# Kernel optimization log

Measured on AMD Instinct MI355X. Metric: run time of the kernel, lower is better.

Reference implementation:

```python
import jax, jax.numpy as jnp
import numpy as np

V, E, HID, K, S = 100000, 256, 512, 20, 4096
HD = HID // 2  # per-direction LSTM hidden
START_ID, STOP_ID = 18, 19


def setup_inputs() -> dict:
    key = jax.random.key(0)
    ks = jax.random.split(key, 14)
    sentence = jax.random.randint(ks[0], (S,), 0, V)
    tags = jax.random.randint(ks[1], (S,), 0, START_ID)  # real tags only
    embed = jax.random.normal(ks[2], (V, E), jnp.float32) * 0.1
    w_ih_f = jax.random.normal(ks[3], (4 * HD, E), jnp.float32) * 0.05
    w_hh_f = jax.random.normal(ks[4], (4 * HD, HD), jnp.float32) * 0.05
    b_f = jax.random.normal(ks[5], (4 * HD,), jnp.float32) * 0.05
    w_ih_b = jax.random.normal(ks[6], (4 * HD, E), jnp.float32) * 0.05
    w_hh_b = jax.random.normal(ks[7], (4 * HD, HD), jnp.float32) * 0.05
    b_b = jax.random.normal(ks[8], (4 * HD,), jnp.float32) * 0.05
    h0 = jax.random.normal(ks[9], (2, HD), jnp.float32)
    c0 = jax.random.normal(ks[10], (2, HD), jnp.float32)
    emit_W = jax.random.normal(ks[11], (K, HID), jnp.float32) * 0.05
    emit_b = jax.random.normal(ks[12], (K,), jnp.float32) * 0.05
    transition = jax.random.normal(ks[13], (K, K), jnp.float32)
    transition = transition.at[START_ID, :].set(-10000.0)
    transition = transition.at[:, STOP_ID].set(-10000.0)
    return dict(sentence=sentence, tags=tags, embed=embed,
                w_ih_f=w_ih_f, w_hh_f=w_hh_f, b_f=b_f,
                w_ih_b=w_ih_b, w_hh_b=w_hh_b, b_b=b_b,
                h0=h0, c0=c0, emit_W=emit_W, emit_b=emit_b,
                transition=transition)


def _lstm_scan(xs, w_ih, w_hh, b, h, c):
    # xs: (S, E); torch gate order i, f, g, o
    def step(carry, x):
        h, c = carry
        z = x @ w_ih.T + h @ w_hh.T + b  # (4*HD,)
        i, f, g, o = jnp.split(z, 4)
        i, f, o = jax.nn.sigmoid(i), jax.nn.sigmoid(f), jax.nn.sigmoid(o)
        g = jnp.tanh(g)
        c = f * c + i * g
        h = o * jnp.tanh(c)
        return (h, c), h
    _, hs = jax.lax.scan(step, (h, c), xs)
    return hs  # (S, HD)


def reference(sentence, tags, embed, w_ih_f, w_hh_f, b_f,
              w_ih_b, w_hh_b, b_b, h0, c0, emit_W, emit_b, transition):
    xs = embed[sentence]  # (S, E)
    h_fwd = _lstm_scan(xs, w_ih_f, w_hh_f, b_f, h0[0], c0[0])
    h_bwd = _lstm_scan(xs[::-1], w_ih_b, w_hh_b, b_b, h0[1], c0[1])[::-1]
    feats = jnp.concatenate([h_fwd, h_bwd], axis=-1) @ emit_W.T + emit_b  # (S, K)

    # CRF forward algorithm (log-partition), tag dim fully vectorized.
    init_fv = jnp.full((K,), -10000.0, feats.dtype).at[START_ID].set(0.0)

    def crf_step(fv, feat):
        # fv_new[next] = logsumexp_prev(fv[prev] + T[next, prev] + feat[next])
        fv = jax.scipy.special.logsumexp(fv[None, :] + transition + feat[:, None], axis=1)
        return fv, None

    fv, _ = jax.lax.scan(crf_step, init_fv, feats)
    log_z = jax.scipy.special.logsumexp(fv + transition[STOP_ID])

    # Gold path score.
    tags_ext = jnp.concatenate([jnp.array([START_ID], tags.dtype), tags])
    gold = (transition[tags_ext[1:], tags_ext[:-1]].sum()
            + feats[jnp.arange(S), tags].sum()
            + transition[STOP_ID, tags[-1]])
    return jnp.stack([log_z, gold])
```

## Files before the change

kernel.cpp:

```cpp
#include <hip/hip_runtime.h>
#include <stdint.h>

#define SLEN 4096
#define EDIM 256
#define HD 256
#define G4 1024
#define KT 20
#define START_ID 18
#define STOP_ID 19

#define NVC 23
#define NLC 9
#define LSTM_LDS_BYTES (1024 + 1024 * NLC * 16)

typedef _Float16 half_t;
typedef _Float16 half2_t __attribute__((ext_vector_type(2)));

__device__ __forceinline__ float dot2(uint32_t w, uint32_t h, float acc) {
#if __has_builtin(__builtin_amdgcn_fdot2)
    return __builtin_amdgcn_fdot2(__builtin_bit_cast(half2_t, w),
                                  __builtin_bit_cast(half2_t, h), acc, false);
#else
    half2_t wv = __builtin_bit_cast(half2_t, w);
    half2_t hv = __builtin_bit_cast(half2_t, h);
    acc += (float)wv.x * (float)hv.x;
    acc += (float)wv.y * (float)hv.y;
    return acc;
#endif
}

__device__ __forceinline__ float fsig(float x) { return 1.f / (1.f + __expf(-x)); }
__device__ __forceinline__ float ftanh(float x) { return 1.f - 2.f / (__expf(2.f * x) + 1.f); }


__global__ __launch_bounds__(256) void k_transpose_ih(const float* __restrict__ wf,
                                                      const float* __restrict__ wb,
                                                      float* __restrict__ wT) {
    __shared__ float tile[32][33];
    int d = blockIdx.z;
    const float* w = d ? wb : wf;
    int ob = blockIdx.x * 32;
    int eb = blockIdx.y * 32;
    int tx = threadIdx.x & 31, ty = threadIdx.x >> 5;
#pragma unroll
    for (int r = 0; r < 32; r += 8)
        tile[ty + r][tx] = w[(long)(ob + ty + r) * EDIM + eb + tx];
    __syncthreads();
    float* dst = wT + (long)d * EDIM * G4;
#pragma unroll
    for (int r = 0; r < 32; r += 8)
        dst[(long)(eb + ty + r) * G4 + ob + tx] = tile[tx][ty + r];
}

__global__ __launch_bounds__(1024) void k_pack_hh(const float* __restrict__ whf,
                                                  const float* __restrict__ whb,
                                                  uint32_t* __restrict__ wpack,
                                                  uint32_t* __restrict__ wtail) {
    int d = blockIdx.y;
    const float* W = d ? whb : whf;
    int t = threadIdx.x;
    int wv = t >> 6, l = t & 63;
    int j = (wv << 4) | (l & 15);
    int g = (l >> 4) & 3;
    int o = g * 256 + j;
    int bx = blockIdx.x;
    if (bx < 92) {
        int k = bx * 2;
        half2_t p = {(half_t)W[(long)o * HD + k], (half_t)W[(long)o * HD + k + 1]};
        wpack[(d * 92 + bx) * 1024 + t] = __builtin_bit_cast(uint32_t, p);
    } else {
        int cb = bx - 92;
        uint32_t q[4];
#pragma unroll
        for (int qq = 0; qq < 4; qq++) {
            int k = 2 * (92 + cb * 4 + qq);
            half2_t p = {(half_t)W[(long)o * HD + k], (half_t)W[(long)o * HD + k + 1]};
            q[qq] = __builtin_bit_cast(uint32_t, p);
        }
        uint4* dst = (uint4*)wtail;
        dst[(d * NLC + cb) * 1024 + t] = make_uint4(q[0], q[1], q[2], q[3]);
    }
}

__global__ __launch_bounds__(256) void k_zx(const int* __restrict__ sentence,
                                            const float* __restrict__ embed,
                                            const float* __restrict__ wT,
                                            const float* __restrict__ bf,
                                            const float* __restrict__ bb,
                                            float* __restrict__ zxp) {
    int d = blockIdx.y;
    int s0 = blockIdx.x * 16;
    const float* bias = d ? bb : bf;
    __shared__ float xbuf[16][EDIM];
    int tid = threadIdx.x;
    for (int r = 0; r < 16; r++) {
        int row = sentence[s0 + r];
        xbuf[r][tid] = embed[(long)row * EDIM + tid];
    }
    __syncthreads();
    const float* wTd = wT + (long)d * EDIM * G4;
    for (int og = 0; og < 4; og++) {
        float acc[16];
#pragma unroll
        for (int r = 0; r < 16; r++) acc[r] = 0.f;
        int o = og * 256 + tid;
        for (int e = 0; e < EDIM; e += 4) {
            float w0 = wTd[(long)(e + 0) * G4 + o];
            float w1 = wTd[(long)(e + 1) * G4 + o];
            float w2 = wTd[(long)(e + 2) * G4 + o];
            float w3 = wTd[(long)(e + 3) * G4 + o];
#pragma unroll
            for (int r = 0; r < 16; r++) {
                float4 x4 = *(const float4*)&xbuf[r][e];
                acc[r] += w0 * x4.x + w1 * x4.y + w2 * x4.z + w3 * x4.w;
            }
        }
        float bv = bias[o];
        int tB = ((tid >> 4) << 6) | (og << 4) | (tid & 15);
#pragma unroll
        for (int r = 0; r < 16; r++)
            zxp[(long)(d * SLEN + s0 + r) * G4 + tB] = acc[r] + bv;
    }
}

__global__ __launch_bounds__(1024, 4) void k_lstm(const float* __restrict__ zxp,
                                                  const uint32_t* __restrict__ wpack,
                                                  const uint4* __restrict__ wtail,
                                                  const float* __restrict__ h0,
                                                  const float* __restrict__ c0,
                                                  float* __restrict__ hs) {
    extern __shared__ char smem[];
    uint4* h2q = (uint4*)smem;
    half_t* h2h = (half_t*)smem;
    uint4* tail = (uint4*)(smem + 1024);

    int d = blockIdx.x;
    int t = threadIdx.x;
    int l = t & 63;
    int j = ((t >> 6) << 4) | (l & 15);

    uint32_t wreg[4 * NVC];
#pragma unroll
    for (int kk = 0; kk < 4 * NVC; kk++) wreg[kk] = wpack[(d * 92 + kk) * 1024 + t];

#pragma unroll
    for (int cb = 0; cb < NLC; cb++)
        tail[cb * 1024 + t] = wtail[(d * NLC + cb) * 1024 + t];

    float c = c0[d * HD + j];
    if (t < 128) {
        half2_t p = {(half_t)h0[d * HD + 2 * t], (half_t)h0[d * HD + 2 * t + 1]};
        ((uint32_t*)h2q)[t] = __builtin_bit_cast(uint32_t, p);
    }
    __syncthreads();

    const float* zxd = zxp + (long)d * SLEN * G4 + t;
    float* hsd = hs + (long)d * SLEN * HD + j;

    float zx_next = zxd[(long)(d ? SLEN - 1 : 0) * G4];

    for (int s = 0; s < SLEN; s++) {
        const int p = s & 1;
        float zx = zx_next;
        if (s + 1 < SLEN) {
            int sxn = d ? (SLEN - 2 - s) : (s + 1);
            zx_next = zxd[(long)sxn * G4];
        }
        const uint4* hq = h2q + p * 32;
        float acc0 = 0.f, acc1 = 0.f;
#pragma unroll
        for (int cc = 0; cc < NVC; cc++) {
            uint4 hv = hq[cc];
            acc0 = dot2(wreg[4 * cc + 0], hv.x, acc0);
            acc1 = dot2(wreg[4 * cc + 1], hv.y, acc1);
            acc0 = dot2(wreg[4 * cc + 2], hv.z, acc0);
            acc1 = dot2(wreg[4 * cc + 3], hv.w, acc1);
        }
#pragma unroll
        for (int cb = 0; cb < NLC; cb++) {
            uint4 tw = tail[cb * 1024 + t];
            uint4 hv = hq[NVC + cb];
            acc0 = dot2(tw.x, hv.x, acc0);
            acc1 = dot2(tw.y, hv.y, acc1);
            acc0 = dot2(tw.z, hv.z, acc0);
            acc1 = dot2(tw.w, hv.w, acc1);
        }
        float z = acc0 + acc1 + zx;
        int lj = l & 15;
        float zi = __shfl(z, lj, 64);
        float zf = __shfl(z, lj + 16, 64);
        float zg = __shfl(z, lj + 32, 64);
        float zo = __shfl(z, lj + 48, 64);
        float ig = fsig(zi), fg = fsig(zf), og = fsig(zo);
        float gg = ftanh(zg);
        c = fg * c + ig * gg;
        float hval = og * ftanh(c);
        if (l < 16) {
            int sx = d ? (SLEN - 1 - s) : s;
            hsd[(long)sx * HD] = hval;
            h2h[((p ^ 1) << 8) + j] = (half_t)hval;
        }
        __syncthreads();
    }
}

__global__ __launch_bounds__(192) void k_feats(const float* __restrict__ hs,
                                               const float* __restrict__ emitW,
                                               const float* __restrict__ emitb,
                                               float* __restrict__ feats) {
    __shared__ float wb[KT][516];
    __shared__ float hb[8][516];
    int tid = threadIdx.x;
    int s0 = blockIdx.x * 8;
    for (int idx = tid; idx < KT * 512; idx += 192) {
        wb[idx >> 9][idx & 511] = emitW[idx];
    }
    for (int idx = tid; idx < 8 * 512; idx += 192) {
        int sl = idx >> 9, jj = idx & 511;
        float v = (jj < 256) ? hs[(long)(s0 + sl) * HD + jj]
                             : hs[(long)(SLEN + s0 + sl) * HD + (jj - 256)];
        hb[sl][jj] = v;
    }
    __syncthreads();
    if (tid < 160) {
        int sl = tid / KT, k = tid % KT;
        float acc = emitb[k];
        for (int jj = 0; jj < 512; jj += 4) {
            float4 wv = *(const float4*)&wb[k][jj];
            float4 hv = *(const float4*)&hb[sl][jj];
            acc += wv.x * hv.x + wv.y * hv.y + wv.z * hv.z + wv.w * hv.w;
        }
        feats[(long)(s0 + sl) * KT + k] = acc;
    }
}

__global__ __launch_bounds__(256) void k_gold(const float* __restrict__ feats,
                                              const int* __restrict__ tags,
                                              const float* __restrict__ trans,
                                              float* __restrict__ out) {
    __shared__ float red[256];
    int tid = threadIdx.x;
    float local = 0.f;
    for (int s2 = tid; s2 < SLEN; s2 += 256) {
        int cur = tags[s2];
        int prev = s2 ? tags[s2 - 1] : START_ID;
        local += trans[cur * KT + prev] + feats[(long)s2 * KT + cur];
    }
    red[tid] = local;
    __syncthreads();
    for (int off = 128; off; off >>= 1) {
        if (tid < off) red[tid] += red[tid + off];
        __syncthreads();
    }
    if (tid == 0) out[1] = red[0] + trans[STOP_ID * KT + tags[SLEN - 1]];
}

__global__ __launch_bounds__(512) void k_crf_chunk(const float* __restrict__ feats,
                                                   const float* __restrict__ trans,
                                                   float* __restrict__ mats) {
    __shared__ float T[KT][KT + 1];
    __shared__ float fb[16][KT];
    __shared__ float cur[2][KT][KT + 1];
    int tid = threadIdx.x;
    int t0 = blockIdx.x * 16;
    if (tid < KT * KT) T[tid / KT][tid % KT] = trans[tid];
    for (int idx = tid; idx < 16 * KT; idx += 512) fb[idx / KT][idx % KT] = feats[(long)t0 * KT + idx];
    __syncthreads();
    int i = tid / KT, jc = tid % KT;
    bool act = tid < KT * KT;
    if (act) cur[0][i][jc] = T[i][jc] + fb[0][i];
    __syncthreads();
    for (int m = 1; m < 16; m++) {
        int p = (m - 1) & 1;
        float nv = 0.f;
        if (act) {
            float vs[KT], vmax = -1e30f;
#pragma unroll
            for (int k = 0; k < KT; k++) { vs[k] = T[i][k] + cur[p][k][jc]; vmax = fmaxf(vmax, vs[k]); }
            float sum = 0.f;
#pragma unroll
            for (int k = 0; k < KT; k++) sum += __expf(vs[k] - vmax);
            nv = fb[m][i] + vmax + __logf(sum);
        }
        if (act) cur[p ^ 1][i][jc] = nv;
        __syncthreads();
    }
    if (act) mats[(long)blockIdx.x * (KT * KT) + tid] = cur[1][i][jc];
}

__global__ __launch_bounds__(512) void k_crf_combine(const float* __restrict__ in,
                                                     float* __restrict__ out_mats,
                                                     int per_block,
                                                     const float* __restrict__ trans,
                                                     float* __restrict__ d_out_ptr,
                                                     int finalize) {
    __shared__ float A[KT][KT + 1];
    __shared__ float cur[2][KT][KT + 1];
    int tid = threadIdx.x;
    int b = blockIdx.x;
    int i = tid / KT, jc = tid % KT;
    bool act = tid < KT * KT;
    const float* base = in + (long)b * per_block * (KT * KT);
    if (act) cur[0][i][jc] = base[tid];
    __syncthreads();
    for (int m = 1; m < per_block; m++) {
        int p = (m - 1) & 1;
        if (act) A[i][jc] = base[(long)m * KT * KT + tid];
        __syncthreads();
        float nv = 0.f;
        if (act) {
            float vs[KT], vmax = -1e30f;
#pragma unroll
            for (int k = 0; k < KT; k++) { vs[k] = A[i][k] + cur[p][k][jc]; vmax = fmaxf(vmax, vs[k]); }
            float sum = 0.f;
#pragma unroll
            for (int k = 0; k < KT; k++) sum += __expf(vs[k] - vmax);
            nv = vmax + __logf(sum);
        }
        if (act) cur[p ^ 1][i][jc] = nv;
        __syncthreads();
    }
    int fbuf = (per_block - 1) & 1;
    if (!finalize) {
        if (act) out_mats[(long)b * KT * KT + tid] = cur[fbuf][i][jc];
        return;
    }
    if (tid == 0) {
        float fv[KT];
        for (int ii = 0; ii < KT; ii++) {
            float vs[KT], vmax = -1e30f;
            for (int k = 0; k < KT; k++) {
                float v = cur[fbuf][ii][k] + (k == START_ID ? 0.f : -10000.f);
                vs[k] = v;
                vmax = fmaxf(vmax, v);
            }
            float sum = 0.f;
            for (int k = 0; k < KT; k++) sum += __expf(vs[k] - vmax);
            fv[ii] = vmax + __logf(sum);
        }
        float vs2[KT], vmax = -1e30f;
        for (int ii = 0; ii < KT; ii++) {
            float v = fv[ii] + trans[STOP_ID * KT + ii];
            vs2[ii] = v;
            vmax = fmaxf(vmax, v);
        }
        float sum = 0.f;
        for (int ii = 0; ii < KT; ii++) sum += __expf(vs2[ii] - vmax);
        d_out_ptr[0] = vmax + __logf(sum);
    }
}

extern "C" void kernel_launch(void* const* d_in, const int* in_sizes, int n_in,
                              void* d_out, int out_size, void* d_ws, size_t ws_size,
                              hipStream_t stream) {
    const int* sentence = (const int*)d_in[0];
    const int* tags = (const int*)d_in[1];
    const float* embed = (const float*)d_in[2];
    const float* w_ih_f = (const float*)d_in[3];
    const float* w_hh_f = (const float*)d_in[4];
    const float* b_f = (const float*)d_in[5];
    const float* w_ih_b = (const float*)d_in[6];
    const float* w_hh_b = (const float*)d_in[7];
    const float* b_b = (const float*)d_in[8];
    const float* h0 = (const float*)d_in[9];
    const float* c0 = (const float*)d_in[10];
    const float* emit_W = (const float*)d_in[11];
    const float* emit_b = (const float*)d_in[12];
    const float* transition = (const float*)d_in[13];
    float* out = (float*)d_out;

    char* ws = (char*)d_ws;
    float* zxp = (float*)(ws + 0);
    float* hs = (float*)(ws + 33554432);
    float* wT = (float*)(ws + 41943040);
    uint32_t* wpack = (uint32_t*)(ws + 44040192);
    uint32_t* wtail = (uint32_t*)(ws + 44793856);
    float* feats = (float*)(ws + 45088768);
    float* mats = (float*)(ws + 45416448);
    float* mats2 = (float*)(ws + 45826048);

    (void)hipFuncSetAttribute((const void*)k_lstm,
                              hipFuncAttributeMaxDynamicSharedMemorySize,
                              LSTM_LDS_BYTES);

    k_transpose_ih<<<dim3(32, 8, 2), 256, 0, stream>>>(w_ih_f, w_ih_b, wT);
    k_pack_hh<<<dim3(101, 2), 1024, 0, stream>>>(w_hh_f, w_hh_b, wpack, wtail);
    k_zx<<<dim3(256, 2), 256, 0, stream>>>(sentence, embed, wT, b_f, b_b, zxp);
    k_lstm<<<dim3(2), 1024, LSTM_LDS_BYTES, stream>>>(zxp, wpack, (const uint4*)wtail, h0, c0, hs);
    k_feats<<<dim3(512), 192, 0, stream>>>(hs, emit_W, emit_b, feats);
    k_gold<<<dim3(1), 256, 0, stream>>>(feats, tags, transition, out);
    k_crf_chunk<<<dim3(256), 512, 0, stream>>>(feats, transition, mats);
    k_crf_combine<<<dim3(16), 512, 0, stream>>>(mats, mats2, 16, transition, out, 0);
    k_crf_combine<<<dim3(1), 512, 0, stream>>>(mats2, nullptr, 16, transition, out, 1);
}
```

Measured before the change: 9.000 ms.

## Halve LSTM block to 512 threads, two gate rows each, broadcast h via readlane

```diff
diff --git a/kernel.cpp b/kernel.cpp
--- a/kernel.cpp
+++ b/kernel.cpp
@@ -16,15 +16,15 @@
 typedef _Float16 half_t;
 typedef _Float16 half2_t __attribute__((ext_vector_type(2)));
 
-__device__ __forceinline__ float dot2(uint32_t w, uint32_t h, float acc) {
+__device__ __forceinline__ float dot2(uint32_t a, uint32_t b, float acc) {
 #if __has_builtin(__builtin_amdgcn_fdot2)
-    return __builtin_amdgcn_fdot2(__builtin_bit_cast(half2_t, w),
-                                  __builtin_bit_cast(half2_t, h), acc, false);
+    return __builtin_amdgcn_fdot2(__builtin_bit_cast(half2_t, a),
+                                  __builtin_bit_cast(half2_t, b), acc, false);
 #else
-    half2_t wv = __builtin_bit_cast(half2_t, w);
-    half2_t hv = __builtin_bit_cast(half2_t, h);
-    acc += (float)wv.x * (float)hv.x;
-    acc += (float)wv.y * (float)hv.y;
+    half2_t av = __builtin_bit_cast(half2_t, a);
+    half2_t bv = __builtin_bit_cast(half2_t, b);
+    acc += (float)av.x * (float)bv.x;
+    acc += (float)av.y * (float)bv.y;
     return acc;
 #endif
 }
@@ -123,84 +123,127 @@
     }
 }
 
-__global__ __launch_bounds__(1024, 4) void k_lstm(const float* __restrict__ zxp,
-                                                  const uint32_t* __restrict__ wpack,
-                                                  const uint4* __restrict__ wtail,
-                                                  const float* __restrict__ h0,
-                                                  const float* __restrict__ c0,
-                                                  float* __restrict__ hs) {
+__global__ __launch_bounds__(512, 2) void k_lstm(const float* __restrict__ zxp,
+                                                 const uint32_t* __restrict__ wpack,
+                                                 const uint4* __restrict__ wtail,
+                                                 const float* __restrict__ h0,
+                                                 const float* __restrict__ c0,
+                                                 float* __restrict__ hs) {
     extern __shared__ char smem[];
-    uint4* h2q = (uint4*)smem;
     half_t* h2h = (half_t*)smem;
+    uint32_t* h2d = (uint32_t*)smem;
     uint4* tail = (uint4*)(smem + 1024);
 
     int d = blockIdx.x;
     int t = threadIdx.x;
     int l = t & 63;
-    int j = ((t >> 6) << 4) | (l & 15);
-
-    uint32_t wreg[4 * NVC];
-#pragma unroll
-    for (int kk = 0; kk < 4 * NVC; kk++) wreg[kk] = wpack[(d * 92 + kk) * 1024 + t];
-
-#pragma unroll
-    for (int cb = 0; cb < NLC; cb++)
+    int w = t >> 6;
+    int lj = l & 15;
+    int j = (w << 4) | lj;
+
+    uint32_t wr1[4 * NVC], wr2[4 * NVC];
+#pragma unroll
+    for (int kk = 0; kk < 4 * NVC; kk++) {
+        wr1[kk] = wpack[(d * 92 + kk) * 1024 + t];
+        wr2[kk] = wpack[(d * 92 + kk) * 1024 + t + 512];
+    }
+#pragma unroll
+    for (int cb = 0; cb < NLC; cb++) {
         tail[cb * 1024 + t] = wtail[(d * NLC + cb) * 1024 + t];
-
-    float c = c0[d * HD + j];
+        tail[cb * 1024 + t + 512] = wtail[(d * NLC + cb) * 1024 + t + 512];
+    }
+
+    float c1 = c0[d * HD + j];
+    float c2 = c0[d * HD + j + 128];
     if (t < 128) {
         half2_t p = {(half_t)h0[d * HD + 2 * t], (half_t)h0[d * HD + 2 * t + 1]};
-        ((uint32_t*)h2q)[t] = __builtin_bit_cast(uint32_t, p);
-    }
-    __syncthreads();
-
-    const float* zxd = zxp + (long)d * SLEN * G4 + t;
-    float* hsd = hs + (long)d * SLEN * HD + j;
-
-    float zx_next = zxd[(long)(d ? SLEN - 1 : 0) * G4];
+        h2d[t] = __builtin_bit_cast(uint32_t, p);
+    }
+    __syncthreads();
+    uint32_t hf0 = h2d[l];
+    uint32_t hf1 = h2d[64 + l];
+
+    const float* zxd = zxp + (long)d * SLEN * G4;
+    float* hsd = hs + (long)d * SLEN * HD;
+
+    int sx0 = d ? (SLEN - 1) : 0;
+    float zx1n = zxd[(long)sx0 * G4 + t];
+    float zx2n = zxd[(long)sx0 * G4 + t + 512];
 
     for (int s = 0; s < SLEN; s++) {
-        const int p = s & 1;
-        float zx = zx_next;
+        float zx1 = zx1n, zx2 = zx2n;
         if (s + 1 < SLEN) {
             int sxn = d ? (SLEN - 2 - s) : (s + 1);
-            zx_next = zxd[(long)sxn * G4];
-        }
-        const uint4* hq = h2q + p * 32;
-        float acc0 = 0.f, acc1 = 0.f;
-#pragma unroll
-        for (int cc = 0; cc < NVC; cc++) {
-            uint4 hv = hq[cc];
-            acc0 = dot2(wreg[4 * cc + 0], hv.x, acc0);
-            acc1 = dot2(wreg[4 * cc + 1], hv.y, acc1);
-            acc0 = dot2(wreg[4 * cc + 2], hv.z, acc0);
-            acc1 = dot2(wreg[4 * cc + 3], hv.w, acc1);
+            zx1n = zxd[(long)sxn * G4 + t];
+            zx2n = zxd[(long)sxn * G4 + t + 512];
+        }
+
+        float a10 = 0.f, a11 = 0.f, a20 = 0.f, a21 = 0.f;
+#pragma unroll
+        for (int kd = 0; kd < 4 * NVC; kd++) {
+            uint32_t hw = (uint32_t)__builtin_amdgcn_readlane(
+                (int)(kd < 64 ? hf0 : hf1), kd & 63);
+            if (kd & 1) {
+                a11 = dot2(hw, wr1[kd], a11);
+                a21 = dot2(hw, wr2[kd], a21);
+            } else {
+                a10 = dot2(hw, wr1[kd], a10);
+                a20 = dot2(hw, wr2[kd], a20);
+            }
         }
 #pragma unroll
         for (int cb = 0; cb < NLC; cb++) {
-            uint4 tw = tail[cb * 1024 + t];
-            uint4 hv = hq[NVC + cb];
-            acc0 = dot2(tw.x, hv.x, acc0);
-            acc1 = dot2(tw.y, hv.y, acc1);
-            acc0 = dot2(tw.z, hv.z, acc0);
-            acc1 = dot2(tw.w, hv.w, acc1);
-        }
-        float z = acc0 + acc1 + zx;
-        int lj = l & 15;
-        float zi = __shfl(z, lj, 64);
-        float zf = __shfl(z, lj + 16, 64);
-        float zg = __shfl(z, lj + 32, 64);
-        float zo = __shfl(z, lj + 48, 64);
-        float ig = fsig(zi), fg = fsig(zf), og = fsig(zo);
-        float gg = ftanh(zg);
-        c = fg * c + ig * gg;
-        float hval = og * ftanh(c);
-        if (l < 16) {
+            uint4 t1 = tail[cb * 1024 + t];
+            uint4 t2 = tail[cb * 1024 + t + 512];
+#pragma unroll
+            for (int qq = 0; qq < 4; qq++) {
+                int kd = 92 + 4 * cb + qq;
+                uint32_t hw = (uint32_t)__builtin_amdgcn_readlane((int)hf1, kd - 64);
+                uint32_t w1v = (qq == 0) ? t1.x : (qq == 1) ? t1.y : (qq == 2) ? t1.z : t1.w;
+                uint32_t w2v = (qq == 0) ? t2.x : (qq == 1) ? t2.y : (qq == 2) ? t2.z : t2.w;
+                if (kd & 1) {
+                    a11 = dot2(hw, w1v, a11);
+                    a21 = dot2(hw, w2v, a21);
+                } else {
+                    a10 = dot2(hw, w1v, a10);
+                    a20 = dot2(hw, w2v, a20);
+                }
+            }
+        }
+
+        float z1 = a10 + a11 + zx1;
+        float z2 = a20 + a21 + zx2;
+
+        float zi1 = __shfl(z1, lj, 64);
+        float zf1 = __shfl(z1, lj + 16, 64);
+        float zg1 = __shfl(z1, lj + 32, 64);
+        float zo1 = __shfl(z1, lj + 48, 64);
+        float zi2 = __shfl(z2, lj, 64);
+        float zf2 = __shfl(z2, lj + 16, 64);
+        float zg2 = __shfl(z2, lj + 32, 64);
+        float zo2 = __shfl(z2, lj + 48, 64);
+
+        float ig1 = fsig(zi1), fg1 = fsig(zf1), og1 = fsig(zo1);
+        float gg1 = ftanh(zg1);
+        c1 = fg1 * c1 + ig1 * gg1;
+        float hv1 = og1 * ftanh(c1);
+
+        float ig2 = fsig(zi2), fg2 = fsig(zf2), og2 = fsig(zo2);
+        float gg2 = ftanh(zg2);
+        c2 = fg2 * c2 + ig2 * gg2;
+        float hv2 = og2 * ftanh(c2);
+
+        int nb = (s & 1) ^ 1;
+        if (l < 32) {
+            int hid = (l < 16) ? j : (j + 128);
+            float hv = (l < 16) ? hv1 : hv2;
             int sx = d ? (SLEN - 1 - s) : s;
-            hsd[(long)sx * HD] = hval;
-            h2h[((p ^ 1) << 8) + j] = (half_t)hval;
+            hsd[(long)sx * HD + hid] = hv;
+            h2h[nb * 256 + hid] = (half_t)hv;
         }
         __syncthreads();
+        hf0 = h2d[nb * 128 + l];
+        hf1 = h2d[nb * 128 + 64 + l];
     }
 }
 
@@ -386,7 +429,7 @@
     k_transpose_ih<<<dim3(32, 8, 2), 256, 0, stream>>>(w_ih_f, w_ih_b, wT);
     k_pack_hh<<<dim3(101, 2), 1024, 0, stream>>>(w_hh_f, w_hh_b, wpack, wtail);
     k_zx<<<dim3(256, 2), 256, 0, stream>>>(sentence, embed, wT, b_f, b_b, zxp);
-    k_lstm<<<dim3(2), 1024, LSTM_LDS_BYTES, stream>>>(zxp, wpack, (const uint4*)wtail, h0, c0, hs);
+    k_lstm<<<dim3(2), 512, LSTM_LDS_BYTES, stream>>>(zxp, wpack, (const uint4*)wtail, h0, c0, hs);
     k_feats<<<dim3(512), 192, 0, stream>>>(hs, emit_W, emit_b, feats);
     k_gold<<<dim3(1), 256, 0, stream>>>(feats, tags, transition, out);
     k_crf_chunk<<<dim3(256), 512, 0, stream>>>(feats, transition, mats);
```

New measurement: 10.75 ms. +19.4%, slower.

## Use MFMA 16x16x32 f16 for LSTM recurrent matvec with repacked weights

Applied to the files above, without the earlier changes.

```diff
diff --git a/kernel.cpp b/kernel.cpp
--- a/kernel.cpp
+++ b/kernel.cpp
@@ -9,25 +9,17 @@
 #define START_ID 18
 #define STOP_ID 19
 
-#define NVC 23
-#define NLC 9
-#define LSTM_LDS_BYTES (1024 + 1024 * NLC * 16)
+#define NT 64
+#define TPW 4
+#define KW 8
+#define NRP 23
+#define NLP 9
+#define LSTM_LDS_BYTES (1024 + 8192 + NLP * 1024 * 16)
 
 typedef _Float16 half_t;
 typedef _Float16 half2_t __attribute__((ext_vector_type(2)));
-
-__device__ __forceinline__ float dot2(uint32_t w, uint32_t h, float acc) {
-#if __has_builtin(__builtin_amdgcn_fdot2)
-    return __builtin_amdgcn_fdot2(__builtin_bit_cast(half2_t, w),
-                                  __builtin_bit_cast(half2_t, h), acc, false);
-#else
-    half2_t wv = __builtin_bit_cast(half2_t, w);
-    half2_t hv = __builtin_bit_cast(half2_t, h);
-    acc += (float)wv.x * (float)hv.x;
-    acc += (float)wv.y * (float)hv.y;
-    return acc;
-#endif
-}
+typedef _Float16 half8 __attribute__((ext_vector_type(8)));
+typedef float f32x4 __attribute__((ext_vector_type(4)));
 
 __device__ __forceinline__ float fsig(float x) { return 1.f / (1.f + __expf(-x)); }
 __device__ __forceinline__ float ftanh(float x) { return 1.f - 2.f / (__expf(2.f * x) + 1.f); }
@@ -52,34 +44,27 @@
         dst[(long)(eb + ty + r) * G4 + ob + tx] = tile[tx][ty + r];
 }
 
-__global__ __launch_bounds__(1024) void k_pack_hh(const float* __restrict__ whf,
-                                                  const float* __restrict__ whb,
-                                                  uint32_t* __restrict__ wpack,
-                                                  uint32_t* __restrict__ wtail) {
-    int d = blockIdx.y;
+__global__ __launch_bounds__(256) void k_pack_mfma(const float* __restrict__ whf,
+                                                   const float* __restrict__ whb,
+                                                   uint4* __restrict__ apack) {
+    int gid = blockIdx.x * 256 + threadIdx.x;
+    int d = gid >> 15;
+    int rem = gid & 32767;
+    int T = rem >> 9;
+    int kw = (rem >> 6) & 7;
+    int l = rem & 63;
     const float* W = d ? whb : whf;
-    int t = threadIdx.x;
-    int wv = t >> 6, l = t & 63;
-    int j = (wv << 4) | (l & 15);
-    int g = (l >> 4) & 3;
-    int o = g * 256 + j;
-    int bx = blockIdx.x;
-    if (bx < 92) {
-        int k = bx * 2;
-        half2_t p = {(half_t)W[(long)o * HD + k], (half_t)W[(long)o * HD + k + 1]};
-        wpack[(d * 92 + bx) * 1024 + t] = __builtin_bit_cast(uint32_t, p);
-    } else {
-        int cb = bx - 92;
-        uint32_t q[4];
-#pragma unroll
-        for (int qq = 0; qq < 4; qq++) {
-            int k = 2 * (92 + cb * 4 + qq);
-            half2_t p = {(half_t)W[(long)o * HD + k], (half_t)W[(long)o * HD + k + 1]};
-            q[qq] = __builtin_bit_cast(uint32_t, p);
-        }
-        uint4* dst = (uint4*)wtail;
-        dst[(d * NLC + cb) * 1024 + t] = make_uint4(q[0], q[1], q[2], q[3]);
-    }
+    int r = T * 16 + (l & 15);
+    int orow = (r & 3) * 256 + (r >> 2);
+    int kbase = kw * 32 + (l >> 4) * 8;
+    uint32_t q[4];
+#pragma unroll
+    for (int dw = 0; dw < 4; dw++) {
+        half2_t p = {(half_t)W[(long)orow * HD + kbase + 2 * dw],
+                     (half_t)W[(long)orow * HD + kbase + 2 * dw + 1]};
+        q[dw] = __builtin_bit_cast(uint32_t, p);
+    }
+    apack[gid] = make_uint4(q[0], q[1], q[2], q[3]);
 }
 
 __global__ __launch_bounds__(256) void k_zx(const int* __restrict__ sentence,
@@ -92,114 +77,126 @@
     int s0 = blockIdx.x * 16;
     const float* bias = d ? bb : bf;
     __shared__ float xbuf[16][EDIM];
-    int tid = threadIdx.x;
+    int u = threadIdx.x;
     for (int r = 0; r < 16; r++) {
         int row = sentence[s0 + r];
-        xbuf[r][tid] = embed[(long)row * EDIM + tid];
+        xbuf[r][u] = embed[(long)row * EDIM + u];
     }
     __syncthreads();
     const float* wTd = wT + (long)d * EDIM * G4;
-    for (int og = 0; og < 4; og++) {
-        float acc[16];
-#pragma unroll
-        for (int r = 0; r < 16; r++) acc[r] = 0.f;
-        int o = og * 256 + tid;
-        for (int e = 0; e < EDIM; e += 4) {
-            float w0 = wTd[(long)(e + 0) * G4 + o];
-            float w1 = wTd[(long)(e + 1) * G4 + o];
-            float w2 = wTd[(long)(e + 2) * G4 + o];
-            float w3 = wTd[(long)(e + 3) * G4 + o];
-#pragma unroll
-            for (int r = 0; r < 16; r++) {
-                float4 x4 = *(const float4*)&xbuf[r][e];
-                acc[r] += w0 * x4.x + w1 * x4.y + w2 * x4.z + w3 * x4.w;
+    float4 a[16];
+    float4 bv = make_float4(bias[u], bias[256 + u], bias[512 + u], bias[768 + u]);
+#pragma unroll
+    for (int r = 0; r < 16; r++) a[r] = bv;
+    for (int e = 0; e < EDIM; e += 4) {
+        float w0[4], w1[4], w2[4], w3[4];
+#pragma unroll
+        for (int k = 0; k < 4; k++) {
+            w0[k] = wTd[(long)(e + k) * G4 + u];
+            w1[k] = wTd[(long)(e + k) * G4 + 256 + u];
+            w2[k] = wTd[(long)(e + k) * G4 + 512 + u];
+            w3[k] = wTd[(long)(e + k) * G4 + 768 + u];
+        }
+#pragma unroll
+        for (int r = 0; r < 16; r++) {
+            float4 x4 = *(const float4*)&xbuf[r][e];
+            float xv[4] = {x4.x, x4.y, x4.z, x4.w};
+#pragma unroll
+            for (int k = 0; k < 4; k++) {
+                a[r].x += w0[k] * xv[k];
+                a[r].y += w1[k] * xv[k];
+                a[r].z += w2[k] * xv[k];
+                a[r].w += w3[k] * xv[k];
             }
         }
-        float bv = bias[o];
-        int tB = ((tid >> 4) << 6) | (og << 4) | (tid & 15);
-#pragma unroll
-        for (int r = 0; r < 16; r++)
-            zxp[(long)(d * SLEN + s0 + r) * G4 + tB] = acc[r] + bv;
-    }
+    }
+#pragma unroll
+    for (int r = 0; r < 16; r++)
+        *(float4*)&zxp[(long)(d * SLEN + s0 + r) * G4 + u * 4] = a[r];
 }
 
 __global__ __launch_bounds__(1024, 4) void k_lstm(const float* __restrict__ zxp,
-                                                  const uint32_t* __restrict__ wpack,
-                                                  const uint4* __restrict__ wtail,
+                                                  const uint4* __restrict__ apack,
                                                   const float* __restrict__ h0,
                                                   const float* __restrict__ c0,
                                                   float* __restrict__ hs) {
     extern __shared__ char smem[];
-    uint4* h2q = (uint4*)smem;
-    half_t* h2h = (half_t*)smem;
-    uint4* tail = (uint4*)(smem + 1024);
+    half_t* hbuf = (half_t*)smem;
+    float* zxl = (float*)(smem + 1024);
+    uint4* tail = (uint4*)(smem + 9216);
 
     int d = blockIdx.x;
     int t = threadIdx.x;
     int l = t & 63;
-    int j = ((t >> 6) << 4) | (l & 15);
-
-    uint32_t wreg[4 * NVC];
-#pragma unroll
-    for (int kk = 0; kk < 4 * NVC; kk++) wreg[kk] = wpack[(d * 92 + kk) * 1024 + t];
-
-#pragma unroll
-    for (int cb = 0; cb < NLC; cb++)
-        tail[cb * 1024 + t] = wtail[(d * NLC + cb) * 1024 + t];
-
-    float c = c0[d * HD + j];
+    int w = t >> 6;
+    int q = l >> 4;
+
+    const uint4* apd = apack + ((long)d * NT + 4 * w) * KW * 64 + l;
+    uint4 areg[NRP];
+#pragma unroll
+    for (int p = 0; p < NRP; p++) areg[p] = apd[p * 64];
+#pragma unroll
+    for (int p = 0; p < NLP; p++) tail[p * 1024 + t] = apd[(NRP + p) * 64];
+
+    float c[TPW];
+#pragma unroll
+    for (int i = 0; i < TPW; i++) c[i] = c0[d * HD + 16 * w + 4 * i + q];
+
     if (t < 128) {
         half2_t p = {(half_t)h0[d * HD + 2 * t], (half_t)h0[d * HD + 2 * t + 1]};
-        ((uint32_t*)h2q)[t] = __builtin_bit_cast(uint32_t, p);
-    }
-    __syncthreads();
-
-    const float* zxd = zxp + (long)d * SLEN * G4 + t;
-    float* hsd = hs + (long)d * SLEN * HD + j;
-
-    float zx_next = zxd[(long)(d ? SLEN - 1 : 0) * G4];
+        ((uint32_t*)hbuf)[t] = __builtin_bit_cast(uint32_t, p);
+    }
+    const float* zxd = zxp + (long)d * SLEN * G4;
+    int sx0 = d ? (SLEN - 1) : 0;
+    if (t < 256) *(float4*)&zxl[t * 4] = *(const float4*)&zxd[(long)sx0 * G4 + t * 4];
+    __syncthreads();
+
+    float* hsd = hs + (long)d * SLEN * HD;
 
     for (int s = 0; s < SLEN; s++) {
         const int p = s & 1;
-        float zx = zx_next;
-        if (s + 1 < SLEN) {
+        f32x4 acc[TPW];
+#pragma unroll
+        for (int i = 0; i < TPW; i++)
+            acc[i] = *(const f32x4*)&zxl[p * 1024 + (4 * w + i) * 16 + q * 4];
+
+        float4 zxn;
+        if (t < 256 && s + 1 < SLEN) {
             int sxn = d ? (SLEN - 2 - s) : (s + 1);
-            zx_next = zxd[(long)sxn * G4];
-        }
-        const uint4* hq = h2q + p * 32;
-        float acc0 = 0.f, acc1 = 0.f;
-#pragma unroll
-        for (int cc = 0; cc < NVC; cc++) {
-            uint4 hv = hq[cc];
-            acc0 = dot2(wreg[4 * cc + 0], hv.x, acc0);
-            acc1 = dot2(wreg[4 * cc + 1], hv.y, acc1);
-            acc0 = dot2(wreg[4 * cc + 2], hv.z, acc0);
-            acc1 = dot2(wreg[4 * cc + 3], hv.w, acc1);
-        }
-#pragma unroll
-        for (int cb = 0; cb < NLC; cb++) {
-            uint4 tw = tail[cb * 1024 + t];
-            uint4 hv = hq[NVC + cb];
-            acc0 = dot2(tw.x, hv.x, acc0);
-            acc1 = dot2(tw.y, hv.y, acc1);
-            acc0 = dot2(tw.z, hv.z, acc0);
-            acc1 = dot2(tw.w, hv.w, acc1);
-        }
-        float z = acc0 + acc1 + zx;
-        int lj = l & 15;
-        float zi = __shfl(z, lj, 64);
-        float zf = __shfl(z, lj + 16, 64);
-        float zg = __shfl(z, lj + 32, 64);
-        float zo = __shfl(z, lj + 48, 64);
-        float ig = fsig(zi), fg = fsig(zf), og = fsig(zo);
-        float gg = ftanh(zg);
-        c = fg * c + ig * gg;
-        float hval = og * ftanh(c);
-        if (l < 16) {
+            zxn = *(const float4*)&zxd[(long)sxn * G4 + t * 4];
+        }
+
+        const half_t* hb = hbuf + p * 256;
+#pragma unroll
+        for (int kw = 0; kw < KW; kw++) {
+            half8 bfrag = *(const half8*)(hb + kw * 32 + q * 8);
+#pragma unroll
+            for (int i = 0; i < TPW; i++) {
+                const int pp = i * KW + kw;
+                uint4 av = (pp < NRP) ? areg[pp] : tail[(pp - NRP) * 1024 + t];
+                acc[i] = __builtin_amdgcn_mfma_f32_16x16x32_f16(
+                    __builtin_bit_cast(half8, av), bfrag, acc[i], 0, 0, 0);
+            }
+        }
+
+        float hv[TPW];
+#pragma unroll
+        for (int i = 0; i < TPW; i++) {
+            float ig = fsig(acc[i][0]), fg = fsig(acc[i][1]);
+            float gg = ftanh(acc[i][2]), og = fsig(acc[i][3]);
+            c[i] = fg * c[i] + ig * gg;
+            hv[i] = og * ftanh(c[i]);
+        }
+
+        int i0 = l & 15;
+        float hvw = (i0 == 0) ? hv[0] : (i0 == 1) ? hv[1] : (i0 == 2) ? hv[2] : hv[3];
+        if (i0 < TPW) {
+            int u = 16 * w + 4 * i0 + q;
             int sx = d ? (SLEN - 1 - s) : s;
-            hsd[(long)sx * HD] = hval;
-            h2h[((p ^ 1) << 8) + j] = (half_t)hval;
-        }
+            hsd[(long)sx * HD + u] = hvw;
+            hbuf[(p ^ 1) * 256 + u] = (half_t)hvw;
+        }
+        if (t < 256 && s + 1 < SLEN) *(float4*)&zxl[(p ^ 1) * 1024 + t * 4] = zxn;
         __syncthreads();
     }
 }
@@ -373,8 +370,7 @@
     float* zxp = (float*)(ws + 0);
     float* hs = (float*)(ws + 33554432);
     float* wT = (float*)(ws + 41943040);
-    uint32_t* wpack = (uint32_t*)(ws + 44040192);
-    uint32_t* wtail = (uint32_t*)(ws + 44793856);
+    uint4* apack = (uint4*)(ws + 44040192);
     float* feats = (float*)(ws + 45088768);
     float* mats = (float*)(ws + 45416448);
     float* mats2 = (float*)(ws + 45826048);
@@ -384,9 +380,9 @@
                               LSTM_LDS_BYTES);
 
     k_transpose_ih<<<dim3(32, 8, 2), 256, 0, stream>>>(w_ih_f, w_ih_b, wT);
-    k_pack_hh<<<dim3(101, 2), 1024, 0, stream>>>(w_hh_f, w_hh_b, wpack, wtail);
+    k_pack_mfma<<<dim3(256), 256, 0, stream>>>(w_hh_f, w_hh_b, apack);
     k_zx<<<dim3(256, 2), 256, 0, stream>>>(sentence, embed, wT, b_f, b_b, zxp);
-    k_lstm<<<dim3(2), 1024, LSTM_LDS_BYTES, stream>>>(zxp, wpack, (const uint4*)wtail, h0, c0, hs);
+    k_lstm<<<dim3(2), 1024, LSTM_LDS_BYTES, stream>>>(zxp, apack, h0, c0, hs);
     k_feats<<<dim3(512), 192, 0, stream>>>(hs, emit_W, emit_b, feats);
     k_gold<<<dim3(1), 256, 0, stream>>>(feats, tags, transition, out);
     k_crf_chunk<<<dim3(256), 512, 0, stream>>>(feats, transition, mats);
```

After: 15.73 ms. +74.8%, slower.

## Split LSTM recurrent matvec over K halves with two gate rows per lane

Applied to the files above, without the earlier changes.

```diff
diff --git a/kernel.cpp b/kernel.cpp
--- a/kernel.cpp
+++ b/kernel.cpp
@@ -9,7 +9,6 @@
 #define START_ID 18
 #define STOP_ID 19
 
-#define NVC 23
 #define NLC 9
 #define LSTM_LDS_BYTES (1024 + 1024 * NLC * 16)
 
@@ -59,26 +58,30 @@
     int d = blockIdx.y;
     const float* W = d ? whb : whf;
     int t = threadIdx.x;
-    int wv = t >> 6, l = t & 63;
-    int j = (wv << 4) | (l & 15);
-    int g = (l >> 4) & 3;
-    int o = g * 256 + j;
+    int l = t & 63;
+    int w = t >> 6;
+    int kh = l >> 5;
+    int gA = (l >> 4) & 1;
+    int j = (w << 4) | (l & 15);
+    int rowA = gA * 256 + j;
+    int rowB = (gA + 2) * 256 + j;
     int bx = blockIdx.x;
+
+    auto packdw = [&](int dd) -> uint32_t {
+        int cc = dd >> 2, qq = dd & 3;
+        int row = (cc < 16) ? rowA : rowB;
+        int k = kh * 128 + (cc & 15) * 8 + qq * 2;
+        half2_t p = {(half_t)W[(long)row * HD + k], (half_t)W[(long)row * HD + k + 1]};
+        return __builtin_bit_cast(uint32_t, p);
+    };
+
     if (bx < 92) {
-        int k = bx * 2;
-        half2_t p = {(half_t)W[(long)o * HD + k], (half_t)W[(long)o * HD + k + 1]};
-        wpack[(d * 92 + bx) * 1024 + t] = __builtin_bit_cast(uint32_t, p);
+        wpack[(d * 92 + bx) * 1024 + t] = packdw(bx);
     } else {
         int cb = bx - 92;
-        uint32_t q[4];
-#pragma unroll
-        for (int qq = 0; qq < 4; qq++) {
-            int k = 2 * (92 + cb * 4 + qq);
-            half2_t p = {(half_t)W[(long)o * HD + k], (half_t)W[(long)o * HD + k + 1]};
-            q[qq] = __builtin_bit_cast(uint32_t, p);
-        }
         uint4* dst = (uint4*)wtail;
-        dst[(d * NLC + cb) * 1024 + t] = make_uint4(q[0], q[1], q[2], q[3]);
+        dst[(d * NLC + cb) * 1024 + t] = make_uint4(packdw(92 + cb * 4), packdw(93 + cb * 4),
+                                                    packdw(94 + cb * 4), packdw(95 + cb * 4));
     }
 }
 
@@ -137,11 +140,15 @@
     int d = blockIdx.x;
     int t = threadIdx.x;
     int l = t & 63;
-    int j = ((t >> 6) << 4) | (l & 15);
-
-    uint32_t wreg[4 * NVC];
-#pragma unroll
-    for (int kk = 0; kk < 4 * NVC; kk++) wreg[kk] = wpack[(d * 92 + kk) * 1024 + t];
+    int w = t >> 6;
+    int kh = l >> 5;
+    int gA = (l >> 4) & 1;
+    int lj = l & 15;
+    int j = (w << 4) | lj;
+
+    uint32_t wreg[92];
+#pragma unroll
+    for (int kk = 0; kk < 92; kk++) wreg[kk] = wpack[(d * 92 + kk) * 1024 + t];
 
 #pragma unroll
     for (int cb = 0; cb < NLC; cb++)
@@ -154,43 +161,58 @@
     }
     __syncthreads();
 
-    const float* zxd = zxp + (long)d * SLEN * G4 + t;
+    const float* zxd = zxp + (long)d * SLEN * G4;
     float* hsd = hs + (long)d * SLEN * HD + j;
-
-    float zx_next = zxd[(long)(d ? SLEN - 1 : 0) * G4];
+    int colA = (w << 6) | (gA << 4) | lj;
+
+    int sx0 = d ? (SLEN - 1) : 0;
+    float zxAn = zxd[(long)sx0 * G4 + colA];
+    float zxBn = zxd[(long)sx0 * G4 + colA + 32];
 
     for (int s = 0; s < SLEN; s++) {
         const int p = s & 1;
-        float zx = zx_next;
+        float zxA = zxAn, zxB = zxBn;
         if (s + 1 < SLEN) {
             int sxn = d ? (SLEN - 2 - s) : (s + 1);
-            zx_next = zxd[(long)sxn * G4];
-        }
-        const uint4* hq = h2q + p * 32;
-        float acc0 = 0.f, acc1 = 0.f;
-#pragma unroll
-        for (int cc = 0; cc < NVC; cc++) {
+            zxAn = zxd[(long)sxn * G4 + colA];
+            zxBn = zxd[(long)sxn * G4 + colA + 32];
+        }
+
+        const uint4* hq = h2q + p * 32 + kh * 16;
+        float pA0 = 0.f, pA1 = 0.f, pB0 = 0.f, pB1 = 0.f;
+#pragma unroll
+        for (int cc = 0; cc < 16; cc++) {
             uint4 hv = hq[cc];
-            acc0 = dot2(wreg[4 * cc + 0], hv.x, acc0);
-            acc1 = dot2(wreg[4 * cc + 1], hv.y, acc1);
-            acc0 = dot2(wreg[4 * cc + 2], hv.z, acc0);
-            acc1 = dot2(wreg[4 * cc + 3], hv.w, acc1);
-        }
-#pragma unroll
-        for (int cb = 0; cb < NLC; cb++) {
-            uint4 tw = tail[cb * 1024 + t];
-            uint4 hv = hq[NVC + cb];
-            acc0 = dot2(tw.x, hv.x, acc0);
-            acc1 = dot2(tw.y, hv.y, acc1);
-            acc0 = dot2(tw.z, hv.z, acc0);
-            acc1 = dot2(tw.w, hv.w, acc1);
-        }
-        float z = acc0 + acc1 + zx;
-        int lj = l & 15;
-        float zi = __shfl(z, lj, 64);
-        float zf = __shfl(z, lj + 16, 64);
-        float zg = __shfl(z, lj + 32, 64);
-        float zo = __shfl(z, lj + 48, 64);
+            pA0 = dot2(wreg[4 * cc + 0], hv.x, pA0);
+            pA1 = dot2(wreg[4 * cc + 1], hv.y, pA1);
+            pA0 = dot2(wreg[4 * cc + 2], hv.z, pA0);
+            pA1 = dot2(wreg[4 * cc + 3], hv.w, pA1);
+            if (cc < 7) {
+                pB0 = dot2(wreg[64 + 4 * cc + 0], hv.x, pB0);
+                pB1 = dot2(wreg[64 + 4 * cc + 1], hv.y, pB1);
+                pB0 = dot2(wreg[64 + 4 * cc + 2], hv.z, pB0);
+                pB1 = dot2(wreg[64 + 4 * cc + 3], hv.w, pB1);
+            } else {
+                uint4 tw = tail[(cc - 7) * 1024 + t];
+                pB0 = dot2(tw.x, hv.x, pB0);
+                pB1 = dot2(tw.y, hv.y, pB1);
+                pB0 = dot2(tw.z, hv.z, pB0);
+                pB1 = dot2(tw.w, hv.w, pB1);
+            }
+        }
+
+        float sA = pA0 + pA1;
+        float sB = pB0 + pB1;
+        sA += __shfl_xor(sA, 32, 64);
+        sB += __shfl_xor(sB, 32, 64);
+        float zAf = sA + zxA;
+        float zBf = sB + zxB;
+
+        float zi = __shfl(zAf, lj, 64);
+        float zf = __shfl(zAf, lj + 16, 64);
+        float zg = __shfl(zBf, lj, 64);
+        float zo = __shfl(zBf, lj + 16, 64);
+
         float ig = fsig(zi), fg = fsig(zf), og = fsig(zo);
         float gg = ftanh(zg);
         c = fg * c + ig * gg;
```

Measured after the change: 8.573 ms. 4.7% less time.
